# Optimization experiments

Measured on AMD Instinct MI355X. Metric: run time of the kernel, lower is better.

## Reference

```python
import jax, jax.numpy as jnp
import numpy as np
from jax import lax

CUTOFF = 0.25
SIGMA = 1.0
RADIUS = 4  # skimage/scipy default truncate=4.0 -> radius = round(4.0*sigma)


def _gauss_kernel(sigma=SIGMA, radius=RADIUS):
    x = np.arange(-radius, radius + 1, dtype=np.float32)
    k = np.exp(-0.5 * (x / sigma) ** 2)
    return jnp.asarray(k / k.sum())


def _blur_axis(x, axis, kernel):
    r = (kernel.shape[0] - 1) // 2
    pad = [(0, 0)] * x.ndim
    pad[axis] = (r, r)
    xp = jnp.pad(x, pad, mode='edge')  # scipy mode='nearest'
    out = jnp.zeros_like(x)
    for i in range(kernel.shape[0]):  # fixed small tap loop (9 taps)
        out = out + kernel[i] * lax.slice_in_dim(xp, i, i + x.shape[axis], axis=axis)
    return out


def gaussian_smoothing_4d(x):
    # skimage.filters.gaussian on a 4D array smooths over ALL axes (B, C, H, W)
    k = _gauss_kernel().astype(x.dtype)
    for ax in range(4):
        x = _blur_axis(x, ax, k)
    return x


def dht_2d(x):
    # real(FFT(x)) - imag(FFT(flip(x)))
    return (jnp.fft.fftn(x, axes=(2, 3)).real
            - jnp.fft.fftn(jnp.flip(x, axis=(2, 3)), axes=(2, 3)).imag).astype(x.dtype)


def _neg_k(a):
    # X_H(-k): flip both spatial mode axes, then roll by 1 (DC stays put)
    return jnp.roll(jnp.flip(a, axis=(-2, -1)), shift=(1, 1), axis=(-2, -1))


def compl_mul2d(x1, x2):
    x1n, x2n = _neg_k(x1), _neg_k(x2)
    e = lambda a, b: jnp.einsum('bixy,ioxy->boxy', a, b)
    return 0.5 * (e(x1, x2) - e(x1n, x2n) + e(x1, x2n) + e(x1n, x2))


def setup_inputs() -> dict:
    key = jax.random.key(0)
    k1, k2 = jax.random.split(key)
    B, Cin, Cout, H, W, M1, M2 = 16, 64, 64, 128, 128, 20, 20
    x = jax.random.normal(k1, (B, Cin, H, W), dtype=jnp.float32)
    scale = 1.0 / (Cin * Cout)
    w1 = scale * jax.random.uniform(k2, (Cin, Cout, M1, M2), dtype=jnp.float32)
    return {'x': x, 'w1': w1}


def reference(x, w1):
    B, _, H, W = x.shape
    Cout, M1, M2 = w1.shape[1], w1.shape[2], w1.shape[3]
    x_ht = dht_2d(x)
    out_ht = jnp.zeros((B, Cout, H, W), dtype=x.dtype)
    out_ht = out_ht.at[:, :, :M1, :M2].set(
        compl_mul2d(x_ht[:, :, :M1, :M2], w1))
    # inverse DHT = DHT / (H*W)
    y = dht_2d(out_ht) / (H * W)
    y = gaussian_smoothing_4d(y)
    # low-pass mask along last dim only (as in the original)
    freqs = jnp.fft.fftfreq(W)
    mask = (jnp.abs(freqs) <= CUTOFF).astype(y.dtype)
    return y * mask
```

## Files before the change

### kernel.cpp

```cpp
#include <hip/hip_runtime.h>


#define TWO_PI 6.283185307179586f
#define THETA (TWO_PI / 128.0f)

__device__ __forceinline__ void gauss9(float* g) {
  float s = 0.f;
#pragma unroll
  for (int t = 0; t < 9; ++t) { float d = (float)(t - 4); g[t] = expf(-0.5f * d * d); s += g[t]; }
  float inv = 1.f / s;
#pragma unroll
  for (int t = 0; t < 9; ++t) g[t] *= inv;
}

__global__ void kA_init(float* __restrict__ L2g, float* __restrict__ RB2g,
                        float* __restrict__ Tg, float* __restrict__ Lf2g,
                        const float* __restrict__ w1, float* __restrict__ wbT) {
  __shared__ float sh[5632];
  int tid = threadIdx.x;
  int blk = blockIdx.x;
  if (blk == 1) {
    for (int i = tid; i < 5120; i += 256) {
      int n2 = i / 40, col = i - n2 * 40;
      int k2 = (col < 20) ? col : col - 20;
      float a = (float)((k2 * n2) & 127) * THETA;
      Tg[i] = (col < 20) ? cosf(a) : sinf(a);
    }
    return;
  }
  if (blk == 2) {
    for (int i = tid; i < 10240; i += 256) {
      int k1 = i >> 9, t = i & 511;
      int q = t >> 7, n1 = t & 127;
      int nn = n1 + ((q >= 2) ? 1 : 0);
      float a = (float)((k1 * nn) & 127) * THETA;
      float v;
      if (q == 0) v = cosf(a);
      else if (q == 1) v = -sinf(a);
      else if (q == 2) v = -sinf(a);
      else v = -cosf(a);
      Lf2g[i] = v;
    }
    return;
  }
  if (blk == 0) {
    for (int i = tid; i < 5376; i += 256) {
      int u = i / 42, t = i - u * 42;
      int A = (t < 21) ? t : t - 21;
      float a = (float)((u * A) & 127) * THETA;
      sh[u * 44 + t] = (t < 21) ? cosf(a) : sinf(a);
    }
    __syncthreads();
    float g[9]; gauss9(g);
    for (int i = tid; i < 5376; i += 256) {
      int u = i / 42, t = i - u * 42;
      float acc = 0.f;
#pragma unroll
      for (int tp = 0; tp < 9; ++tp) {
        int uc = u - 4 + tp; uc = uc < 0 ? 0 : (uc > 127 ? 127 : uc);
        acc += g[tp] * sh[uc * 44 + t];
      }
      L2g[t * 128 + u] = acc;
      bool keep = (u <= 32) || (u >= 96);
      RB2g[t * 128 + u] = keep ? acc : 0.f;
    }
    return;
  }
  int bb = blk - 3;
  int c = bb / 7, chunk = bb % 7;
  int m0 = chunk * 64;
  int mw = 400 - m0; if (mw > 64) mw = 64;
  for (int t = tid; t < 4096; t += 256) {
    int o = t >> 6, mm = t & 63;
    sh[o * 69 + mm] = (mm < mw) ? w1[(c * 64 + o) * 400 + m0 + mm] : 0.f;
  }
  __syncthreads();
  float g[9]; gauss9(g);
  for (int t = tid; t < 4096; t += 256) {
    int mm = t >> 6, o = t & 63;
    if (mm >= mw) continue;
    float acc = 0.f;
#pragma unroll
    for (int tp = 0; tp < 9; ++tp) {
      int oc = o - 4 + tp; oc = oc < 0 ? 0 : (oc > 63 ? 63 : oc);
      acc += g[tp] * sh[oc * 69 + mm];
    }
    wbT[(c * 400 + m0 + mm) * 64 + o] = acc;
  }
}

__global__ void __launch_bounds__(320, 5) k12(const float* __restrict__ x,
                                              const float* __restrict__ Tg,
                                              const float* __restrict__ Lf2g,
                                              float* __restrict__ X1) {
  __shared__ float lds[8448];
  int bc = blockIdx.x, tid = threadIdx.x;
  int w = __builtin_amdgcn_readfirstlane(tid >> 6);
  int L = tid & 63;
  const float* xb = x + (long)bc * 16384;
  const float* tgw = Tg + w * 8;

  float acc[2][8];
#pragma unroll
  for (int i = 0; i < 2; ++i)
#pragma unroll
    for (int j = 0; j < 8; ++j) acc[i][j] = 0.f;

  float4 pv[7];
#pragma unroll
  for (int i = 0; i < 7; ++i) {
    int t = tid + 320 * i;
    if (t < 2048) {
      int n2l = t & 63, n1g = t >> 6;
      const float* gp = xb + n1g * 512 + n2l;
      pv[i] = make_float4(gp[0], gp[128], gp[256], gp[384]);
    }
  }
  for (int ch = 0; ch < 2; ++ch) {
    __syncthreads();
#pragma unroll
    for (int i = 0; i < 7; ++i) {
      int t = tid + 320 * i;
      if (t < 2048) {
        int n2l = t & 63, n1g = t >> 6;
        *(float4*)&lds[n2l * 132 + n1g * 4] = pv[i];
      }
    }
    if (ch == 0) {
#pragma unroll
      for (int i = 0; i < 7; ++i) {
        int t = tid + 320 * i;
        if (t < 2048) {
          int n2l = t & 63, n1g = t >> 6;
          const float* gp = xb + n1g * 512 + 64 + n2l;
          pv[i] = make_float4(gp[0], gp[128], gp[256], gp[384]);
        }
      }
    }
    __syncthreads();
#pragma unroll 4
    for (int k = 0; k < 64; ++k) {
      float2 av = *(const float2*)&lds[k * 132 + 2 * L];
      const float* tr = tgw + (ch * 64 + k) * 40;
      float4 b0 = *(const float4*)tr;
      float4 b1 = *(const float4*)(tr + 4);
      float bv[8] = {b0.x, b0.y, b0.z, b0.w, b1.x, b1.y, b1.z, b1.w};
#pragma unroll
      for (int j = 0; j < 8; ++j) {
        acc[0][j] += av.x * bv[j];
        acc[1][j] += av.y * bv[j];
      }
    }
  }
  __syncthreads();
#pragma unroll
  for (int j = 0; j < 8; ++j) {
    int col = w * 8 + j;
    int k2 = (col < 20) ? col : col - 20;
    int part = (col < 20) ? 0 : 128;
    int m = (k2 & 7) << 2;
    *(float2*)&lds[k2 * 256 + ((part + 2 * L) ^ m)] =
        make_float2(acc[0][j], acc[1][j]);
  }
  __syncthreads();
  if (tid < 200) {
    int k1 = tid / 10, k2 = (tid % 10) * 2;
    int m0 = (k2 & 7) << 2, m1 = ((k2 + 1) & 7) << 2;
    const float* lrow = Lf2g + k1 * 512;
    const float* p0 = lds + k2 * 256;
    const float* p1 = lds + (k2 + 1) * 256;
    float d0a = 0.f, d1a = 0.f, d2ca = 0.f, d2sa = 0.f, d3ca = 0.f, d3sa = 0.f;
    float d0b = 0.f, d1b = 0.f, d2cb = 0.f, d2sb = 0.f, d3cb = 0.f, d3sb = 0.f;
    for (int t = 0; t < 128; t += 4) {
      float4 l0 = *(const float4*)(lrow + t);
      float4 l1 = *(const float4*)(lrow + 128 + t);
      float4 l2 = *(const float4*)(lrow + 256 + t);
      float4 l3 = *(const float4*)(lrow + 384 + t);
      float4 pc0 = *(const float4*)(p0 + (t ^ m0));
      float4 ps0 = *(const float4*)(p0 + ((128 + t) ^ m0));
      float4 pc1 = *(const float4*)(p1 + (t ^ m1));
      float4 ps1 = *(const float4*)(p1 + ((128 + t) ^ m1));
      d0a += l0.x*pc0.x + l0.y*pc0.y + l0.z*pc0.z + l0.w*pc0.w;
      d1a += l1.x*ps0.x + l1.y*ps0.y + l1.z*ps0.z + l1.w*ps0.w;
      d2ca += l2.x*pc0.x + l2.y*pc0.y + l2.z*pc0.z + l2.w*pc0.w;
      d2sa += l2.x*ps0.x + l2.y*ps0.y + l2.z*ps0.z + l2.w*ps0.w;
      d3ca += l3.x*pc0.x + l3.y*pc0.y + l3.z*pc0.z + l3.w*pc0.w;
      d3sa += l3.x*ps0.x + l3.y*ps0.y + l3.z*ps0.z + l3.w*ps0.w;
      d0b += l0.x*pc1.x + l0.y*pc1.y + l0.z*pc1.z + l0.w*pc1.w;
      d1b += l1.x*ps1.x + l1.y*ps1.y + l1.z*ps1.z + l1.w*ps1.w;
      d2cb += l2.x*pc1.x + l2.y*pc1.y + l2.z*pc1.z + l2.w*pc1.w;
      d2sb += l2.x*ps1.x + l2.y*ps1.y + l2.z*ps1.z + l2.w*ps1.w;
      d3cb += l3.x*pc1.x + l3.y*pc1.y + l3.z*pc1.z + l3.w*pc1.w;
      d3sb += l3.x*ps1.x + l3.y*ps1.y + l3.z*ps1.z + l3.w*ps1.w;
    }
    float ska, cka, skb, ckb;
    sincosf(THETA * (float)k2, &ska, &cka);
    sincosf(THETA * (float)(k2 + 1), &skb, &ckb);
    X1[(k1 * 20 + k2) * 1024 + bc] = d0a + d1a + cka * (d2ca + d3sa) + ska * (d3ca - d2sa);
    X1[(k1 * 20 + k2 + 1) * 1024 + bc] = d0b + d1b + ckb * (d2cb + d3sb) + skb * (d3cb - d2sb);
  }
}

__global__ void k3_mix(const float* __restrict__ X1, const float* __restrict__ wbT,
                       float* __restrict__ O) {
  __shared__ float Xp[16][64], Xm[16][64];
  int m = blockIdx.x;
  int i = m / 20, j = m - i * 20;
  int nm = ((20 - i) % 20) * 20 + ((20 - j) % 20);
  int tid = threadIdx.x;
  const float sc = 0.5f / 16384.0f;
  float g[9]; gauss9(g);
  {
    int bl = tid >> 6, c = tid & 63;
#pragma unroll
    for (int it = 0; it < 4; ++it) {
      int b = bl * 4 + it;
      float sa = 0.f, sn = 0.f;
#pragma unroll
      for (int tp = 0; tp < 9; ++tp) {
        int bb = b - 4 + tp; bb = bb < 0 ? 0 : (bb > 15 ? 15 : bb);
        sa += g[tp] * X1[m * 1024 + bb * 64 + c];
        sn += g[tp] * X1[nm * 1024 + bb * 64 + c];
      }
      Xp[b][c] = (sa + sn) * sc; Xm[b][c] = (sa - sn) * sc;
    }
  }
  __syncthreads();
  int o = tid & 63, bq = tid >> 6;
  float acc[4] = {0.f, 0.f, 0.f, 0.f};
#pragma unroll 4
  for (int c = 0; c < 64; ++c) {
    float wp = wbT[(c * 400 + m) * 64 + o];
    float wm = wbT[(c * 400 + nm) * 64 + o];
#pragma unroll
    for (int k = 0; k < 4; ++k)
      acc[k] += Xp[bq * 4 + k][c] * wp + Xm[bq * 4 + k][c] * wm;
  }
#pragma unroll
  for (int k = 0; k < 4; ++k)
    O[((bq * 4 + k) * 64 + o) * 400 + m] = acc[k];
}

__global__ void __launch_bounds__(256) k5b_final(const float* __restrict__ O,
                                                 const float* __restrict__ L2g,
                                                 const float* __restrict__ RB2g,
                                                 float* __restrict__ out) {
  __shared__ float Os[400];
  __shared__ float Rs[42 * 128];
  int bo = blockIdx.x, tid = threadIdx.x;
  for (int t = tid; t < 400; t += 256) Os[t] = O[bo * 400 + t];
  __syncthreads();
  const float4* Bc4 = (const float4*)RB2g;
  const float4* Bs4 = (const float4*)(RB2g + 21 * 128);
  {
    int rg = tid & 7;
    int vqIdx = tid >> 3;
    int vq = (vqIdx < 9) ? vqIdx : vqIdx + 15;
    if (rg < 7 && vqIdx < 17) {
      int r0 = rg * 6;
      float4 a[6];
#pragma unroll
      for (int q = 0; q < 6; ++q) a[q] = make_float4(0.f, 0.f, 0.f, 0.f);
      for (int k2 = 0; k2 <= 20; ++k2) {
        float4 bc = Bc4[k2 * 32 + vq];
        float4 bs = Bs4[k2 * 32 + vq];
#pragma unroll
        for (int q = 0; q < 6; ++q) {
          int r = r0 + q;
          bool isS = (r >= 21);
          int A = isS ? (r - 21) : r;
          if (k2 < 20 && A < 20) {
            float ov = Os[A * 20 + k2];
            const float4 b = isS ? bs : bc;
            float s = isS ? -ov : ov;
            a[q].x += s * b.x; a[q].y += s * b.y; a[q].z += s * b.z; a[q].w += s * b.w;
          }
          if (k2 >= 1 && A >= 1) {
            float ov = Os[(A - 1) * 20 + (k2 - 1)];
            const float4 b = isS ? bc : bs;
            a[q].x -= ov * b.x; a[q].y -= ov * b.y; a[q].z -= ov * b.z; a[q].w -= ov * b.w;
          }
        }
      }
#pragma unroll
      for (int q = 0; q < 6; ++q)
        *(float4*)&Rs[(r0 + q) * 128 + vq * 4] = a[q];
    }
  }
  __syncthreads();
  long base = (long)bo * 16384;
  {
    int half = tid >> 7;
    int uu = (tid >> 3) & 15;  int u0 = uu * 8;
    int vv = tid & 7;          int v0 = half ? (96 + vv * 4) : vv * 4;
    float acc[8][4];
#pragma unroll
    for (int a = 0; a < 8; ++a)
#pragma unroll
      for (int b = 0; b < 4; ++b) acc[a][b] = 0.f;
    for (int r = 0; r < 42; ++r) {
      float4 a0 = *(const float4*)(L2g + r * 128 + u0);
      float4 a1 = *(const float4*)(L2g + r * 128 + u0 + 4);
      float4 b0 = *(const float4*)&Rs[r * 128 + v0];
      float av[8] = {a0.x, a0.y, a0.z, a0.w, a1.x, a1.y, a1.z, a1.w};
      float bv[4] = {b0.x, b0.y, b0.z, b0.w};
#pragma unroll
      for (int a = 0; a < 8; ++a)
#pragma unroll
        for (int b = 0; b < 4; ++b) acc[a][b] += av[a] * bv[b];
    }
#pragma unroll
    for (int a = 0; a < 8; ++a)
      *(float4*)&out[base + (u0 + a) * 128 + v0] =
          make_float4(acc[a][0], acc[a][1], acc[a][2], acc[a][3]);
  }
  if (tid < 128) {
    float d = 0.f;
    for (int r = 0; r < 42; ++r) d += L2g[r * 128 + tid] * Rs[r * 128 + 32];
    out[base + tid * 128 + 32] = d;
  }
  float4 z4 = make_float4(0.f, 0.f, 0.f, 0.f);
  for (int jj = tid; jj < 2048; jj += 256) {
    int u = jj >> 4, s = jj & 15;
    long p = base + (long)u * 128;
    if (s == 15) { out[p + 33] = 0.f; out[p + 34] = 0.f; out[p + 35] = 0.f; }
    else *(float4*)&out[p + 36 + 4 * s] = z4;
  }
}

extern "C" void kernel_launch(void* const* d_in, const int* in_sizes, int n_in,
                              void* d_out, int out_size, void* d_ws, size_t ws_size,
                              hipStream_t stream) {
  const float* x = (const float*)d_in[0];
  const float* w1 = (const float*)d_in[1];
  float* out = (float*)d_out;
  float* ws = (float*)d_ws;

  float* X1 = ws;
  float* O = X1 + 409600;
  float* wbT = O + 409600;
  float* Tg = wbT + 1638400;
  float* Lf2g = Tg + 5120;
  float* L2g = Lf2g + 10240;
  float* RB2g = L2g + 5376;

  hipLaunchKernelGGL(kA_init, dim3(451), dim3(256), 0, stream,
                     L2g, RB2g, Tg, Lf2g, w1, wbT);
  hipLaunchKernelGGL(k12, dim3(1024), dim3(320), 0, stream, x, Tg, Lf2g, X1);
  hipLaunchKernelGGL(k3_mix, dim3(400), dim3(256), 0, stream, X1, wbT, O);
  hipLaunchKernelGGL(k5b_final, dim3(1024), dim3(256), 0, stream, O, L2g, RB2g, out);
}
```

Baseline: 208.4 us.

## Fuse four kernels into one cooperative kernel with grid-wide syncs

```diff
diff --git a/kernel.cpp b/kernel.cpp
--- a/kernel.cpp
+++ b/kernel.cpp
@@ -1,4 +1,7 @@
 #include <hip/hip_runtime.h>
+#include <hip/hip_cooperative_groups.h>
+
+namespace cg = cooperative_groups;
 
 
 #define TWO_PI 6.283185307179586f
@@ -13,318 +16,292 @@
   for (int t = 0; t < 9; ++t) g[t] *= inv;
 }
 
-__global__ void kA_init(float* __restrict__ L2g, float* __restrict__ RB2g,
-                        float* __restrict__ Tg, float* __restrict__ Lf2g,
-                        const float* __restrict__ w1, float* __restrict__ wbT) {
-  __shared__ float sh[5632];
+__global__ void __launch_bounds__(256, 4) fused(
+    const float* __restrict__ x, const float* __restrict__ w1,
+    float* __restrict__ out, float* __restrict__ X1, float* __restrict__ O,
+    float* __restrict__ wbT, float* __restrict__ Tg, float* __restrict__ Lf2g,
+    float* __restrict__ L2g, float* __restrict__ RB2g, int phase) {
+  __shared__ float lds[5776];
+  cg::grid_group grid = cg::this_grid();
+  const bool all = (phase < 0);
   int tid = threadIdx.x;
   int blk = blockIdx.x;
-  if (blk == 1) {
-    for (int i = tid; i < 5120; i += 256) {
-      int n2 = i / 40, col = i - n2 * 40;
+
+  if (all || phase == 0) {
+    if (blk == 1) {
+      for (int i = tid; i < 5120; i += 256) {
+        int n2 = i / 40, col = i - n2 * 40;
+        int k2 = (col < 20) ? col : col - 20;
+        float a = (float)((k2 * n2) & 127) * THETA;
+        Tg[i] = (col < 20) ? cosf(a) : sinf(a);
+      }
+    } else if (blk == 2) {
+      for (int i = tid; i < 10240; i += 256) {
+        int k1 = i >> 9, t = i & 511;
+        int q = t >> 7, n1 = t & 127;
+        int nn = n1 + ((q >= 2) ? 1 : 0);
+        float a = (float)((k1 * nn) & 127) * THETA;
+        float v;
+        if (q == 0) v = cosf(a);
+        else if (q == 1) v = -sinf(a);
+        else if (q == 2) v = -sinf(a);
+        else v = -cosf(a);
+        Lf2g[i] = v;
+      }
+    } else if (blk == 0) {
+      for (int i = tid; i < 5376; i += 256) {
+        int u = i / 42, t = i - u * 42;
+        int A = (t < 21) ? t : t - 21;
+        float a = (float)((u * A) & 127) * THETA;
+        lds[u * 44 + t] = (t < 21) ? cosf(a) : sinf(a);
+      }
+      __syncthreads();
+      float g[9]; gauss9(g);
+      for (int i = tid; i < 5376; i += 256) {
+        int u = i / 42, t = i - u * 42;
+        float acc = 0.f;
+#pragma unroll
+        for (int tp = 0; tp < 9; ++tp) {
+          int uc = u - 4 + tp; uc = uc < 0 ? 0 : (uc > 127 ? 127 : uc);
+          acc += g[tp] * lds[uc * 44 + t];
+        }
+        L2g[t * 128 + u] = acc;
+        bool keep = (u <= 32) || (u >= 96);
+        RB2g[t * 128 + u] = keep ? acc : 0.f;
+      }
+    } else if (blk < 451) {
+      int bb = blk - 3;
+      int c = bb / 7, chunk = bb % 7;
+      int m0 = chunk * 64;
+      int mw = 400 - m0; if (mw > 64) mw = 64;
+      for (int t = tid; t < 4096; t += 256) {
+        int o = t >> 6, mm = t & 63;
+        lds[o * 69 + mm] = (mm < mw) ? w1[(c * 64 + o) * 400 + m0 + mm] : 0.f;
+      }
+      __syncthreads();
+      float g[9]; gauss9(g);
+      for (int t = tid; t < 4096; t += 256) {
+        int mm = t >> 6, o = t & 63;
+        if (mm >= mw) continue;
+        float acc = 0.f;
+#pragma unroll
+        for (int tp = 0; tp < 9; ++tp) {
+          int oc = o - 4 + tp; oc = oc < 0 ? 0 : (oc > 63 ? 63 : oc);
+          acc += g[tp] * lds[oc * 69 + mm];
+        }
+        wbT[(c * 400 + m0 + mm) * 64 + o] = acc;
+      }
+    }
+  }
+  if (all) grid.sync();
+
+  if (all || phase == 1) {
+    int bc = blk;
+    const float* xb = x + (long)bc * 16384;
+    int w = __builtin_amdgcn_readfirstlane(tid >> 6);
+    int L = tid & 63;
+    const float* tgw = Tg + w * 10;
+    float acc[2][10];
+#pragma unroll
+    for (int i = 0; i < 2; ++i)
+#pragma unroll
+      for (int j = 0; j < 10; ++j) acc[i][j] = 0.f;
+
+    for (int ch = 0; ch < 4; ++ch) {
+      __syncthreads();
+      for (int t = tid; t < 1024; t += 256) {
+        int n2l = t & 31, n1g = t >> 5;
+        const float* gp = xb + n1g * 512 + ch * 32 + n2l;
+        float4 v = make_float4(gp[0], gp[128], gp[256], gp[384]);
+        *(float4*)&lds[n2l * 132 + n1g * 4] = v;
+      }
+      __syncthreads();
+#pragma unroll 4
+      for (int k = 0; k < 32; ++k) {
+        float2 av = *(const float2*)&lds[k * 132 + 2 * L];
+        const float* tr = tgw + (ch * 32 + k) * 40;
+        float bv[10];
+#pragma unroll
+        for (int j = 0; j < 10; ++j) bv[j] = tr[j];
+#pragma unroll
+        for (int j = 0; j < 10; ++j) {
+          acc[0][j] += av.x * bv[j];
+          acc[1][j] += av.y * bv[j];
+        }
+      }
+    }
+    __syncthreads();
+#pragma unroll
+    for (int j = 0; j < 10; ++j) {
+      int col = w * 10 + j;
       int k2 = (col < 20) ? col : col - 20;
-      float a = (float)((k2 * n2) & 127) * THETA;
-      Tg[i] = (col < 20) ? cosf(a) : sinf(a);
-    }
-    return;
-  }
-  if (blk == 2) {
-    for (int i = tid; i < 10240; i += 256) {
-      int k1 = i >> 9, t = i & 511;
-      int q = t >> 7, n1 = t & 127;
-      int nn = n1 + ((q >= 2) ? 1 : 0);
-      float a = (float)((k1 * nn) & 127) * THETA;
-      float v;
-      if (q == 0) v = cosf(a);
-      else if (q == 1) v = -sinf(a);
-      else if (q == 2) v = -sinf(a);
-      else v = -cosf(a);
-      Lf2g[i] = v;
-    }
-    return;
-  }
-  if (blk == 0) {
-    for (int i = tid; i < 5376; i += 256) {
-      int u = i / 42, t = i - u * 42;
-      int A = (t < 21) ? t : t - 21;
-      float a = (float)((u * A) & 127) * THETA;
-      sh[u * 44 + t] = (t < 21) ? cosf(a) : sinf(a);
-    }
-    __syncthreads();
+      int part = (col < 20) ? 0 : 128;
+      int m = (k2 & 7) << 2;
+      *(float2*)&lds[k2 * 256 + ((part + 2 * L) ^ m)] =
+          make_float2(acc[0][j], acc[1][j]);
+    }
+    __syncthreads();
+    if (tid < 200) {
+      int k1 = tid / 10, k2 = (tid % 10) * 2;
+      int m0 = (k2 & 7) << 2, m1 = ((k2 + 1) & 7) << 2;
+      const float* lrow = Lf2g + k1 * 512;
+      const float* p0 = lds + k2 * 256;
+      const float* p1 = lds + (k2 + 1) * 256;
+      float d0a = 0.f, d1a = 0.f, d2ca = 0.f, d2sa = 0.f, d3ca = 0.f, d3sa = 0.f;
+      float d0b = 0.f, d1b = 0.f, d2cb = 0.f, d2sb = 0.f, d3cb = 0.f, d3sb = 0.f;
+      for (int t = 0; t < 128; t += 4) {
+        float4 l0 = *(const float4*)(lrow + t);
+        float4 l1 = *(const float4*)(lrow + 128 + t);
+        float4 l2 = *(const float4*)(lrow + 256 + t);
+        float4 l3 = *(const float4*)(lrow + 384 + t);
+        float4 pc0 = *(const float4*)(p0 + (t ^ m0));
+        float4 ps0 = *(const float4*)(p0 + ((128 + t) ^ m0));
+        float4 pc1 = *(const float4*)(p1 + (t ^ m1));
+        float4 ps1 = *(const float4*)(p1 + ((128 + t) ^ m1));
+        d0a += l0.x*pc0.x + l0.y*pc0.y + l0.z*pc0.z + l0.w*pc0.w;
+        d1a += l1.x*ps0.x + l1.y*ps0.y + l1.z*ps0.z + l1.w*ps0.w;
+        d2ca += l2.x*pc0.x + l2.y*pc0.y + l2.z*pc0.z + l2.w*pc0.w;
+        d2sa += l2.x*ps0.x + l2.y*ps0.y + l2.z*ps0.z + l2.w*ps0.w;
+        d3ca += l3.x*pc0.x + l3.y*pc0.y + l3.z*pc0.z + l3.w*pc0.w;
+        d3sa += l3.x*ps0.x + l3.y*ps0.y + l3.z*ps0.z + l3.w*ps0.w;
+        d0b += l0.x*pc1.x + l0.y*pc1.y + l0.z*pc1.z + l0.w*pc1.w;
+        d1b += l1.x*ps1.x + l1.y*ps1.y + l1.z*ps1.z + l1.w*ps1.w;
+        d2cb += l2.x*pc1.x + l2.y*pc1.y + l2.z*pc1.z + l2.w*pc1.w;
+        d2sb += l2.x*ps1.x + l2.y*ps1.y + l2.z*ps1.z + l2.w*ps1.w;
+        d3cb += l3.x*pc1.x + l3.y*pc1.y + l3.z*pc1.z + l3.w*pc1.w;
+        d3sb += l3.x*ps1.x + l3.y*ps1.y + l3.z*ps1.z + l3.w*ps1.w;
+      }
+      float ska, cka, skb, ckb;
+      sincosf(THETA * (float)k2, &ska, &cka);
+      sincosf(THETA * (float)(k2 + 1), &skb, &ckb);
+      X1[(k1 * 20 + k2) * 1024 + bc] = d0a + d1a + cka * (d2ca + d3sa) + ska * (d3ca - d2sa);
+      X1[(k1 * 20 + k2 + 1) * 1024 + bc] = d0b + d1b + ckb * (d2cb + d3sb) + skb * (d3cb - d2sb);
+    }
+  }
+  if (all) grid.sync();
+
+  if ((all || phase == 2) && blk < 400) {
+    float (*Xp)[64] = (float(*)[64])lds;
+    float (*Xm)[64] = (float(*)[64])(lds + 1024);
+    int m = blk;
+    int i = m / 20, j = m - i * 20;
+    int nm = ((20 - i) % 20) * 20 + ((20 - j) % 20);
+    const float sc = 0.5f / 16384.0f;
     float g[9]; gauss9(g);
-    for (int i = tid; i < 5376; i += 256) {
-      int u = i / 42, t = i - u * 42;
-      float acc = 0.f;
-#pragma unroll
-      for (int tp = 0; tp < 9; ++tp) {
-        int uc = u - 4 + tp; uc = uc < 0 ? 0 : (uc > 127 ? 127 : uc);
-        acc += g[tp] * sh[uc * 44 + t];
-      }
-      L2g[t * 128 + u] = acc;
-      bool keep = (u <= 32) || (u >= 96);
-      RB2g[t * 128 + u] = keep ? acc : 0.f;
-    }
-    return;
-  }
-  int bb = blk - 3;
-  int c = bb / 7, chunk = bb % 7;
-  int m0 = chunk * 64;
-  int mw = 400 - m0; if (mw > 64) mw = 64;
-  for (int t = tid; t < 4096; t += 256) {
-    int o = t >> 6, mm = t & 63;
-    sh[o * 69 + mm] = (mm < mw) ? w1[(c * 64 + o) * 400 + m0 + mm] : 0.f;
-  }
-  __syncthreads();
-  float g[9]; gauss9(g);
-  for (int t = tid; t < 4096; t += 256) {
-    int mm = t >> 6, o = t & 63;
-    if (mm >= mw) continue;
-    float acc = 0.f;
-#pragma unroll
-    for (int tp = 0; tp < 9; ++tp) {
-      int oc = o - 4 + tp; oc = oc < 0 ? 0 : (oc > 63 ? 63 : oc);
-      acc += g[tp] * sh[oc * 69 + mm];
-    }
-    wbT[(c * 400 + m0 + mm) * 64 + o] = acc;
-  }
-}
-
-__global__ void __launch_bounds__(320, 5) k12(const float* __restrict__ x,
-                                              const float* __restrict__ Tg,
-                                              const float* __restrict__ Lf2g,
-                                              float* __restrict__ X1) {
-  __shared__ float lds[8448];
-  int bc = blockIdx.x, tid = threadIdx.x;
-  int w = __builtin_amdgcn_readfirstlane(tid >> 6);
-  int L = tid & 63;
-  const float* xb = x + (long)bc * 16384;
-  const float* tgw = Tg + w * 8;
-
-  float acc[2][8];
-#pragma unroll
-  for (int i = 0; i < 2; ++i)
-#pragma unroll
-    for (int j = 0; j < 8; ++j) acc[i][j] = 0.f;
-
-  float4 pv[7];
-#pragma unroll
-  for (int i = 0; i < 7; ++i) {
-    int t = tid + 320 * i;
-    if (t < 2048) {
-      int n2l = t & 63, n1g = t >> 6;
-      const float* gp = xb + n1g * 512 + n2l;
-      pv[i] = make_float4(gp[0], gp[128], gp[256], gp[384]);
-    }
-  }
-  for (int ch = 0; ch < 2; ++ch) {
-    __syncthreads();
-#pragma unroll
-    for (int i = 0; i < 7; ++i) {
-      int t = tid + 320 * i;
-      if (t < 2048) {
-        int n2l = t & 63, n1g = t >> 6;
-        *(float4*)&lds[n2l * 132 + n1g * 4] = pv[i];
-      }
-    }
-    if (ch == 0) {
-#pragma unroll
-      for (int i = 0; i < 7; ++i) {
-        int t = tid + 320 * i;
-        if (t < 2048) {
-          int n2l = t & 63, n1g = t >> 6;
-          const float* gp = xb + n1g * 512 + 64 + n2l;
-          pv[i] = make_float4(gp[0], gp[128], gp[256], gp[384]);
-        }
-      }
-    }
-    __syncthreads();
+    {
+      int bl = tid >> 6, c = tid & 63;
+#pragma unroll
+      for (int it = 0; it < 4; ++it) {
+        int b = bl * 4 + it;
+        float sa = 0.f, sn = 0.f;
+#pragma unroll
+        for (int tp = 0; tp < 9; ++tp) {
+          int bb = b - 4 + tp; bb = bb < 0 ? 0 : (bb > 15 ? 15 : bb);
+          sa += g[tp] * X1[m * 1024 + bb * 64 + c];
+          sn += g[tp] * X1[nm * 1024 + bb * 64 + c];
+        }
+        Xp[b][c] = (sa + sn) * sc; Xm[b][c] = (sa - sn) * sc;
+      }
+    }
+    __syncthreads();
+    int o = tid & 63, bq = tid >> 6;
+    float acc[4] = {0.f, 0.f, 0.f, 0.f};
 #pragma unroll 4
-    for (int k = 0; k < 64; ++k) {
-      float2 av = *(const float2*)&lds[k * 132 + 2 * L];
-      const float* tr = tgw + (ch * 64 + k) * 40;
-      float4 b0 = *(const float4*)tr;
-      float4 b1 = *(const float4*)(tr + 4);
-      float bv[8] = {b0.x, b0.y, b0.z, b0.w, b1.x, b1.y, b1.z, b1.w};
-#pragma unroll
-      for (int j = 0; j < 8; ++j) {
-        acc[0][j] += av.x * bv[j];
-        acc[1][j] += av.y * bv[j];
-      }
-    }
-  }
-  __syncthreads();
-#pragma unroll
-  for (int j = 0; j < 8; ++j) {
-    int col = w * 8 + j;
-    int k2 = (col < 20) ? col : col - 20;
-    int part = (col < 20) ? 0 : 128;
-    int m = (k2 & 7) << 2;
-    *(float2*)&lds[k2 * 256 + ((part + 2 * L) ^ m)] =
-        make_float2(acc[0][j], acc[1][j]);
-  }
-  __syncthreads();
-  if (tid < 200) {
-    int k1 = tid / 10, k2 = (tid % 10) * 2;
-    int m0 = (k2 & 7) << 2, m1 = ((k2 + 1) & 7) << 2;
-    const float* lrow = Lf2g + k1 * 512;
-    const float* p0 = lds + k2 * 256;
-    const float* p1 = lds + (k2 + 1) * 256;
-    float d0a = 0.f, d1a = 0.f, d2ca = 0.f, d2sa = 0.f, d3ca = 0.f, d3sa = 0.f;
-    float d0b = 0.f, d1b = 0.f, d2cb = 0.f, d2sb = 0.f, d3cb = 0.f, d3sb = 0.f;
-    for (int t = 0; t < 128; t += 4) {
-      float4 l0 = *(const float4*)(lrow + t);
-      float4 l1 = *(const float4*)(lrow + 128 + t);
-      float4 l2 = *(const float4*)(lrow + 256 + t);
-      float4 l3 = *(const float4*)(lrow + 384 + t);
-      float4 pc0 = *(const float4*)(p0 + (t ^ m0));
-      float4 ps0 = *(const float4*)(p0 + ((128 + t) ^ m0));
-      float4 pc1 = *(const float4*)(p1 + (t ^ m1));
-      float4 ps1 = *(const float4*)(p1 + ((128 + t) ^ m1));
-      d0a += l0.x*pc0.x + l0.y*pc0.y + l0.z*pc0.z + l0.w*pc0.w;
-      d1a += l1.x*ps0.x + l1.y*ps0.y + l1.z*ps0.z + l1.w*ps0.w;
-      d2ca += l2.x*pc0.x + l2.y*pc0.y + l2.z*pc0.z + l2.w*pc0.w;
-      d2sa += l2.x*ps0.x + l2.y*ps0.y + l2.z*ps0.z + l2.w*ps0.w;
-      d3ca += l3.x*pc0.x + l3.y*pc0.y + l3.z*pc0.z + l3.w*pc0.w;
-      d3sa += l3.x*ps0.x + l3.y*ps0.y + l3.z*ps0.z + l3.w*ps0.w;
-      d0b += l0.x*pc1.x + l0.y*pc1.y + l0.z*pc1.z + l0.w*pc1.w;
-      d1b += l1.x*ps1.x + l1.y*ps1.y + l1.z*ps1.z + l1.w*ps1.w;
-      d2cb += l2.x*pc1.x + l2.y*pc1.y + l2.z*pc1.z + l2.w*pc1.w;
-      d2sb += l2.x*ps1.x + l2.y*ps1.y + l2.z*ps1.z + l2.w*ps1.w;
-      d3cb += l3.x*pc1.x + l3.y*pc1.y + l3.z*pc1.z + l3.w*pc1.w;
-      d3sb += l3.x*ps1.x + l3.y*ps1.y + l3.z*ps1.z + l3.w*ps1.w;
-    }
-    float ska, cka, skb, ckb;
-    sincosf(THETA * (float)k2, &ska, &cka);
-    sincosf(THETA * (float)(k2 + 1), &skb, &ckb);
-    X1[(k1 * 20 + k2) * 1024 + bc] = d0a + d1a + cka * (d2ca + d3sa) + ska * (d3ca - d2sa);
-    X1[(k1 * 20 + k2 + 1) * 1024 + bc] = d0b + d1b + ckb * (d2cb + d3sb) + skb * (d3cb - d2sb);
-  }
-}
-
-__global__ void k3_mix(const float* __restrict__ X1, const float* __restrict__ wbT,
-                       float* __restrict__ O) {
-  __shared__ float Xp[16][64], Xm[16][64];
-  int m = blockIdx.x;
-  int i = m / 20, j = m - i * 20;
-  int nm = ((20 - i) % 20) * 20 + ((20 - j) % 20);
-  int tid = threadIdx.x;
-  const float sc = 0.5f / 16384.0f;
-  float g[9]; gauss9(g);
-  {
-    int bl = tid >> 6, c = tid & 63;
-#pragma unroll
-    for (int it = 0; it < 4; ++it) {
-      int b = bl * 4 + it;
-      float sa = 0.f, sn = 0.f;
-#pragma unroll
-      for (int tp = 0; tp < 9; ++tp) {
-        int bb = b - 4 + tp; bb = bb < 0 ? 0 : (bb > 15 ? 15 : bb);
-        sa += g[tp] * X1[m * 1024 + bb * 64 + c];
-        sn += g[tp] * X1[nm * 1024 + bb * 64 + c];
-      }
-      Xp[b][c] = (sa + sn) * sc; Xm[b][c] = (sa - sn) * sc;
-    }
-  }
-  __syncthreads();
-  int o = tid & 63, bq = tid >> 6;
-  float acc[4] = {0.f, 0.f, 0.f, 0.f};
-#pragma unroll 4
-  for (int c = 0; c < 64; ++c) {
-    float wp = wbT[(c * 400 + m) * 64 + o];
-    float wm = wbT[(c * 400 + nm) * 64 + o];
+    for (int c = 0; c < 64; ++c) {
+      float wp = wbT[(c * 400 + m) * 64 + o];
+      float wm = wbT[(c * 400 + nm) * 64 + o];
+#pragma unroll
+      for (int k = 0; k < 4; ++k)
+        acc[k] += Xp[bq * 4 + k][c] * wp + Xm[bq * 4 + k][c] * wm;
+    }
 #pragma unroll
     for (int k = 0; k < 4; ++k)
-      acc[k] += Xp[bq * 4 + k][c] * wp + Xm[bq * 4 + k][c] * wm;
-  }
-#pragma unroll
-  for (int k = 0; k < 4; ++k)
-    O[((bq * 4 + k) * 64 + o) * 400 + m] = acc[k];
-}
-
-__global__ void __launch_bounds__(256) k5b_final(const float* __restrict__ O,
-                                                 const float* __restrict__ L2g,
-                                                 const float* __restrict__ RB2g,
-                                                 float* __restrict__ out) {
-  __shared__ float Os[400];
-  __shared__ float Rs[42 * 128];
-  int bo = blockIdx.x, tid = threadIdx.x;
-  for (int t = tid; t < 400; t += 256) Os[t] = O[bo * 400 + t];
-  __syncthreads();
-  const float4* Bc4 = (const float4*)RB2g;
-  const float4* Bs4 = (const float4*)(RB2g + 21 * 128);
-  {
-    int rg = tid & 7;
-    int vqIdx = tid >> 3;
-    int vq = (vqIdx < 9) ? vqIdx : vqIdx + 15;
-    if (rg < 7 && vqIdx < 17) {
-      int r0 = rg * 6;
-      float4 a[6];
-#pragma unroll
-      for (int q = 0; q < 6; ++q) a[q] = make_float4(0.f, 0.f, 0.f, 0.f);
-      for (int k2 = 0; k2 <= 20; ++k2) {
-        float4 bc = Bc4[k2 * 32 + vq];
-        float4 bs = Bs4[k2 * 32 + vq];
-#pragma unroll
-        for (int q = 0; q < 6; ++q) {
-          int r = r0 + q;
-          bool isS = (r >= 21);
-          int A = isS ? (r - 21) : r;
-          if (k2 < 20 && A < 20) {
-            float ov = Os[A * 20 + k2];
-            const float4 b = isS ? bs : bc;
-            float s = isS ? -ov : ov;
-            a[q].x += s * b.x; a[q].y += s * b.y; a[q].z += s * b.z; a[q].w += s * b.w;
+      O[((bq * 4 + k) * 64 + o) * 400 + m] = acc[k];
+  }
+  if (all) grid.sync();
+
+  if (all || phase == 3) {
+    float* Os = lds;
+    float* Rs = lds + 400;
+    int bo = blk;
+    for (int t = tid; t < 400; t += 256) Os[t] = O[bo * 400 + t];
+    __syncthreads();
+    const float4* Bc4 = (const float4*)RB2g;
+    const float4* Bs4 = (const float4*)(RB2g + 21 * 128);
+    {
+      int rg = tid & 7;
+      int vqIdx = tid >> 3;
+      int vq = (vqIdx < 9) ? vqIdx : vqIdx + 15;
+      if (rg < 7 && vqIdx < 17) {
+        int r0 = rg * 6;
+        float4 a[6];
+#pragma unroll
+        for (int q = 0; q < 6; ++q) a[q] = make_float4(0.f, 0.f, 0.f, 0.f);
+        for (int k2 = 0; k2 <= 20; ++k2) {
+          float4 bc4 = Bc4[k2 * 32 + vq];
+          float4 bs4 = Bs4[k2 * 32 + vq];
+#pragma unroll
+          for (int q = 0; q < 6; ++q) {
+            int r = r0 + q;
+            bool isS = (r >= 21);
+            int A = isS ? (r - 21) : r;
+            if (k2 < 20 && A < 20) {
+              float ov = Os[A * 20 + k2];
+              const float4 b = isS ? bs4 : bc4;
+              float s = isS ? -ov : ov;
+              a[q].x += s * b.x; a[q].y += s * b.y; a[q].z += s * b.z; a[q].w += s * b.w;
+            }
+            if (k2 >= 1 && A >= 1) {
+              float ov = Os[(A - 1) * 20 + (k2 - 1)];
+              const float4 b = isS ? bc4 : bs4;
+              a[q].x -= ov * b.x; a[q].y -= ov * b.y; a[q].z -= ov * b.z; a[q].w -= ov * b.w;
+            }
           }
-          if (k2 >= 1 && A >= 1) {
-            float ov = Os[(A - 1) * 20 + (k2 - 1)];
-            const float4 b = isS ? bc : bs;
-            a[q].x -= ov * b.x; a[q].y -= ov * b.y; a[q].z -= ov * b.z; a[q].w -= ov * b.w;
-          }
-        }
-      }
-#pragma unroll
-      for (int q = 0; q < 6; ++q)
-        *(float4*)&Rs[(r0 + q) * 128 + vq * 4] = a[q];
-    }
-  }
-  __syncthreads();
-  long base = (long)bo * 16384;
-  {
-    int half = tid >> 7;
-    int uu = (tid >> 3) & 15;  int u0 = uu * 8;
-    int vv = tid & 7;          int v0 = half ? (96 + vv * 4) : vv * 4;
-    float acc[8][4];
-#pragma unroll
-    for (int a = 0; a < 8; ++a)
-#pragma unroll
-      for (int b = 0; b < 4; ++b) acc[a][b] = 0.f;
-    for (int r = 0; r < 42; ++r) {
-      float4 a0 = *(const float4*)(L2g + r * 128 + u0);
-      float4 a1 = *(const float4*)(L2g + r * 128 + u0 + 4);
-      float4 b0 = *(const float4*)&Rs[r * 128 + v0];
-      float av[8] = {a0.x, a0.y, a0.z, a0.w, a1.x, a1.y, a1.z, a1.w};
-      float bv[4] = {b0.x, b0.y, b0.z, b0.w};
+        }
+#pragma unroll
+        for (int q = 0; q < 6; ++q)
+          *(float4*)&Rs[(r0 + q) * 128 + vq * 4] = a[q];
+      }
+    }
+    __syncthreads();
+    long base = (long)bo * 16384;
+    {
+      int half = tid >> 7;
+      int uu = (tid >> 3) & 15;  int u0 = uu * 8;
+      int vv = tid & 7;          int v0 = half ? (96 + vv * 4) : vv * 4;
+      float acc[8][4];
 #pragma unroll
       for (int a = 0; a < 8; ++a)
 #pragma unroll
-        for (int b = 0; b < 4; ++b) acc[a][b] += av[a] * bv[b];
-    }
-#pragma unroll
-    for (int a = 0; a < 8; ++a)
-      *(float4*)&out[base + (u0 + a) * 128 + v0] =
-          make_float4(acc[a][0], acc[a][1], acc[a][2], acc[a][3]);
-  }
-  if (tid < 128) {
-    float d = 0.f;
-    for (int r = 0; r < 42; ++r) d += L2g[r * 128 + tid] * Rs[r * 128 + 32];
-    out[base + tid * 128 + 32] = d;
-  }
-  float4 z4 = make_float4(0.f, 0.f, 0.f, 0.f);
-  for (int jj = tid; jj < 2048; jj += 256) {
-    int u = jj >> 4, s = jj & 15;
-    long p = base + (long)u * 128;
-    if (s == 15) { out[p + 33] = 0.f; out[p + 34] = 0.f; out[p + 35] = 0.f; }
-    else *(float4*)&out[p + 36 + 4 * s] = z4;
+        for (int b = 0; b < 4; ++b) acc[a][b] = 0.f;
+      for (int r = 0; r < 42; ++r) {
+        float4 a0 = *(const float4*)(L2g + r * 128 + u0);
+        float4 a1 = *(const float4*)(L2g + r * 128 + u0 + 4);
+        float4 b0 = *(const float4*)&Rs[r * 128 + v0];
+        float av[8] = {a0.x, a0.y, a0.z, a0.w, a1.x, a1.y, a1.z, a1.w};
+        float bv[4] = {b0.x, b0.y, b0.z, b0.w};
+#pragma unroll
+        for (int a = 0; a < 8; ++a)
+#pragma unroll
+          for (int b = 0; b < 4; ++b) acc[a][b] += av[a] * bv[b];
+      }
+#pragma unroll
+      for (int a = 0; a < 8; ++a)
+        *(float4*)&out[base + (u0 + a) * 128 + v0] =
+            make_float4(acc[a][0], acc[a][1], acc[a][2], acc[a][3]);
+    }
+    if (tid < 128) {
+      float d = 0.f;
+      for (int r = 0; r < 42; ++r) d += L2g[r * 128 + tid] * Rs[r * 128 + 32];
+      out[base + tid * 128 + 32] = d;
+    }
+    float4 z4 = make_float4(0.f, 0.f, 0.f, 0.f);
+    for (int jj = tid; jj < 2048; jj += 256) {
+      int u = jj >> 4, s = jj & 15;
+      long p = base + (long)u * 128;
+      if (s == 15) { out[p + 33] = 0.f; out[p + 34] = 0.f; out[p + 35] = 0.f; }
+      else *(float4*)&out[p + 36 + 4 * s] = z4;
+    }
   }
 }
 
@@ -344,9 +321,15 @@
   float* L2g = Lf2g + 10240;
   float* RB2g = L2g + 5376;
 
-  hipLaunchKernelGGL(kA_init, dim3(451), dim3(256), 0, stream,
-                     L2g, RB2g, Tg, Lf2g, w1, wbT);
-  hipLaunchKernelGGL(k12, dim3(1024), dim3(320), 0, stream, x, Tg, Lf2g, X1);
-  hipLaunchKernelGGL(k3_mix, dim3(400), dim3(256), 0, stream, X1, wbT, O);
-  hipLaunchKernelGGL(k5b_final, dim3(1024), dim3(256), 0, stream, O, L2g, RB2g, out);
+  int phase = -1;
+  void* args[] = {(void*)&x, (void*)&w1, (void*)&out, (void*)&X1, (void*)&O,
+                  (void*)&wbT, (void*)&Tg, (void*)&Lf2g, (void*)&L2g,
+                  (void*)&RB2g, (void*)&phase};
+  hipError_t err = hipLaunchCooperativeKernel((const void*)fused, dim3(1024),
+                                              dim3(256), args, 0, stream);
+  if (err != hipSuccess) {
+    for (int p = 0; p < 4; ++p)
+      hipLaunchKernelGGL(fused, dim3(1024), dim3(256), 0, stream,
+                         x, w1, out, X1, O, wbT, Tg, Lf2g, L2g, RB2g, p);
+  }
 }
```

Result: slower. 606.0 us (+190.8%).
